# Performance work log

Measured on AMD Instinct MI355X. Metric: run time of the kernel, lower is better.

The kernel has to match this reference:

```python
import jax, jax.numpy as jnp
import numpy as np

EMBED_DIM = 512
NUM_TYPES = 26
PER_TYPE = 128
NUM_CODES = NUM_TYPES * PER_TYPE
COMMIT = 0.25
TEMP = 0.07
N_TOKENS = 32768
SAMPLED_PER_TYPE = int(0.1 * PER_TYPE)  # 12


def _normalize(v, axis=-1):
    # matches F.normalize(p=2) with eps clamp
    return v / jnp.clip(jnp.linalg.norm(v, axis=axis, keepdims=True), 1e-12)


def setup_inputs() -> dict:
    key = jax.random.key(0)
    k1, k2, k3, k4 = jax.random.split(key, 4)
    x = jax.random.normal(k1, (N_TOKENS, EMBED_DIM), jnp.float32)
    Q = jax.random.randint(k2, (N_TOKENS,), 0, NUM_TYPES)
    initrange = 1.0 / EMBED_DIM
    emb = jax.random.uniform(k3, (NUM_CODES, EMBED_DIM), jnp.float32, -initrange, initrange)
    emb = _normalize(emb)  # mirrors _initialize_embeddings
    # deterministic stand-in for torch.randperm(num_per_type)[:sampled_num]
    perm = jax.random.permutation(k4, PER_TYPE)[:SAMPLED_PER_TYPE]
    sampled_indices = (jnp.arange(NUM_TYPES)[:, None] * PER_TYPE + perm[None, :]).reshape(-1)
    return {"x": x, "embeddings": emb, "Q": Q, "sampled_indices": sampled_indices}


def _code_indices(xn, embeddings, Q):
    # full [N, num_codes] squared distances, then select the 128-code slab of
    # each token's PTM type and argmin within it (equivalent to the per-type loop)
    d = ((xn ** 2).sum(-1, keepdims=True)
         + (embeddings ** 2).sum(-1)[None, :]
         - 2.0 * (xn @ embeddings.T))                      # [N, NUM_CODES]
    d = d.reshape(xn.shape[0], NUM_TYPES, PER_TYPE)
    d_sel = jnp.take_along_axis(d, Q[:, None, None], axis=1)[:, 0, :]  # [N, PER_TYPE]
    return jnp.argmin(d_sel, axis=1) + Q * PER_TYPE


def _uniform_loss(embeddings, sampled_indices):
    ne = _normalize(embeddings)
    se = ne[sampled_indices]                               # [S, D]
    sim = se @ se.T                                        # [S, S]
    labels = sampled_indices // PER_TYPE
    pos = (labels[None, :] == labels[:, None]).astype(jnp.float32)
    S = sampled_indices.shape[0]
    eye = jnp.eye(S, dtype=bool)
    sim = jnp.where(eye, -jnp.inf, sim)
    sim_exp = jnp.exp(sim / TEMP)                          # exp(-inf) = 0 kills diagonal
    sum_exp = sim_exp.sum(axis=1)
    pos_sum = (sim_exp * pos).sum(axis=1)
    return -jnp.log(pos_sum / sum_exp).mean()


def reference(x, embeddings, Q, sampled_indices):
    xn = _normalize(x)
    idx = _code_indices(xn, embeddings, Q)
    quantized = _normalize(embeddings[idx])
    q_latent = jnp.mean((quantized - jax.lax.stop_gradient(xn)) ** 2)
    e_latent = jnp.mean((xn - jax.lax.stop_gradient(quantized)) ** 2)
    loss = q_latent + COMMIT * e_latent
    uloss = _uniform_loss(embeddings, sampled_indices)
    out = xn + jax.lax.stop_gradient(quantized - xn)       # straight-through
    return out, loss, uloss, idx
```

## Files before the change

### kernel.cpp

```cpp
#include <hip/hip_runtime.h>
#include <math.h>

#define NTOK   32768
#define DIM    512
#define NTYPES 26
#define PT     128
#define NCODES 3328
#define NSAMP  312
#define INV_TEMP (1.0f / 0.07f)
#define MAXTILES 24

typedef __attribute__((ext_vector_type(8))) short short8;
typedef __attribute__((ext_vector_type(4))) float floatx4;

__device__ __forceinline__ void f2bf2(float f, unsigned short& h, unsigned short& l) {
    unsigned u = __float_as_uint(f);
    unsigned hb = (u + 0x7fffu + ((u >> 16) & 1u)) >> 16;
    h = (unsigned short)hb;
    float hf = __uint_as_float(hb << 16);
    float r = f - hf;
    unsigned u2 = __float_as_uint(r);
    l = (unsigned short)((u2 + 0x7fffu + ((u2 >> 16) & 1u)) >> 16);
}

__global__ __launch_bounds__(256) void k_emb(const float* __restrict__ emb,
                                             unsigned short* __restrict__ Bhg,
                                             unsigned short* __restrict__ Blg,
                                             float* __restrict__ sume,
                                             float* __restrict__ rinv,
                                             int* __restrict__ counts,
                                             float* __restrict__ accg) {
    int tid = threadIdx.x;
    if (blockIdx.x == 0) {
        if (tid < NTYPES) counts[tid] = 0;
        if (tid == 32) accg[0] = 0.0f;
        if (tid == 33) accg[1] = 0.0f;
    }
    int wv = tid >> 6, lane = tid & 63;
    int c = blockIdx.x * 4 + wv;
    const float4* row = (const float4*)(emb + (size_t)c * DIM);
    float4 v0 = row[lane * 2], v1 = row[lane * 2 + 1];
    float s = v0.x*v0.x + v0.y*v0.y + v0.z*v0.z + v0.w*v0.w
            + v1.x*v1.x + v1.y*v1.y + v1.z*v1.z + v1.w*v1.w;
    for (int m = 32; m; m >>= 1) s += __shfl_xor(s, m);
    if (lane == 0) {
        sume[c] = s;
        rinv[c] = 1.0f / fmaxf(sqrtf(s), 1e-12f);
    }
    union { short8 v; unsigned short u[8]; } hh, ll;
    f2bf2(v0.x, hh.u[0], ll.u[0]); f2bf2(v0.y, hh.u[1], ll.u[1]);
    f2bf2(v0.z, hh.u[2], ll.u[2]); f2bf2(v0.w, hh.u[3], ll.u[3]);
    f2bf2(v1.x, hh.u[4], ll.u[4]); f2bf2(v1.y, hh.u[5], ll.u[5]);
    f2bf2(v1.z, hh.u[6], ll.u[6]); f2bf2(v1.w, hh.u[7], ll.u[7]);
    *(short8*)(Bhg + (size_t)c * DIM + lane * 8) = hh.v;
    *(short8*)(Blg + (size_t)c * DIM + lane * 8) = ll.v;
}

__global__ __launch_bounds__(256) void k_hist(const int* __restrict__ Q,
                                              int* __restrict__ counts,
                                              int* __restrict__ rank) {
    __shared__ int lbin[NTYPES];
    __shared__ int lbase[NTYPES];
    int tid = threadIdx.x;
    if (tid < NTYPES) lbin[tid] = 0;
    __syncthreads();
    int t = blockIdx.x * 256 + tid;
    int qt = Q[t];
    int lr = atomicAdd(&lbin[qt], 1);
    __syncthreads();
    if (tid < NTYPES) lbase[tid] = atomicAdd(&counts[tid], lbin[tid]);
    __syncthreads();
    rank[t] = lbase[qt] + lr;
}

__global__ __launch_bounds__(256) void k_scatter(const int* __restrict__ Q,
                                                 const int* __restrict__ counts,
                                                 const int* __restrict__ rank,
                                                 int* __restrict__ order,
                                                 int* __restrict__ offsg) {
    __shared__ int offs[NTYPES];
    int tid = threadIdx.x;
    if (tid == 0) {
        int a = 0;
        for (int i = 0; i < NTYPES; i++) {
            offs[i] = a;
            if (blockIdx.x == 0) offsg[i] = a;
            a += counts[i];
        }
        if (blockIdx.x == 0) offsg[NTYPES] = a;
    }
    __syncthreads();
    int t = blockIdx.x * 256 + tid;
    order[offs[Q[t]] + rank[t]] = t;
}

__global__ __launch_bounds__(256, 3) void k_main(const float* __restrict__ x,
                                                 const float* __restrict__ emb,
                                                 const unsigned short* __restrict__ Bhg,
                                                 const unsigned short* __restrict__ Blg,
                                                 const int* __restrict__ order,
                                                 const int* __restrict__ offsg,
                                                 const float* __restrict__ sume,
                                                 const float* __restrict__ rinv,
                                                 float* __restrict__ outbuf,
                                                 float* __restrict__ idxout,
                                                 float* __restrict__ accg) {
    int q = blockIdx.x;
    int tile = blockIdx.y;
    int base = offsg[q];
    int cnt = offsg[q + 1] - base;
    int tstart = tile * 64;
    if (tstart >= cnt) return;
    int nt = min(64, cnt - tstart);

    __shared__ unsigned short Ah[64][72];
    __shared__ unsigned short Al[64][72];
    __shared__ unsigned short Bh[128 * 64];
    __shared__ unsigned short Bl[128 * 64];
    __shared__ int   toks_s[64];
    __shared__ float rn_s[64];
    __shared__ float sume_s[128];
    __shared__ float rinv_s[128];
    __shared__ float redv[64][2];
    __shared__ int   redi[64][2];
    __shared__ int   bestc[64];

    int tid = threadIdx.x;
    int lane = tid & 63;
    int wv = tid >> 6;
    int wm = wv & 1, wn = wv >> 1;
    int lc = lane & 15;
    int q4 = lane >> 4;

    if (tid < 64) toks_s[tid] = order[base + tstart + min(tid, nt - 1)];
    if (tid < 128) {
        sume_s[tid] = sume[q * PT + tid];
        rinv_s[tid] = rinv[q * PT + tid];
    }

    floatx4 acc[2][4];
#pragma unroll
    for (int mi = 0; mi < 2; mi++)
#pragma unroll
        for (int ni = 0; ni < 4; ni++)
            acc[mi][ni] = (floatx4){0.f, 0.f, 0.f, 0.f};
    float ps[4] = {0.f, 0.f, 0.f, 0.f};

    const unsigned short* bh_slab = Bhg + (size_t)q * PT * DIM;
    const unsigned short* bl_slab = Blg + (size_t)q * PT * DIM;

    for (int kc = 0; kc < 8; kc++) {
        int k0 = kc * 64;
        __syncthreads();
#pragma unroll
        for (int i = 0; i < 4; i++) {
            int id = tid + i * 256;
            int r = id >> 4, sg = id & 15;
            float4 v = *(const float4*)(x + (size_t)toks_s[r] * DIM + k0 + sg * 4);
            ps[i] = fmaf(v.x, v.x, fmaf(v.y, v.y, fmaf(v.z, v.z, fmaf(v.w, v.w, ps[i]))));
            ushort4 h, l;
            f2bf2(v.x, h.x, l.x); f2bf2(v.y, h.y, l.y);
            f2bf2(v.z, h.z, l.z); f2bf2(v.w, h.w, l.w);
            *(ushort4*)&Ah[r][sg * 4] = h;
            *(ushort4*)&Al[r][sg * 4] = l;
        }
#pragma unroll
        for (int i = 0; i < 4; i++) {
            int id = tid + i * 256;
            int r = id >> 3, p = id & 7;
            int dst = r * 64 + ((p ^ (r & 7)) << 3);
            *(short8*)&Bh[dst] = *(const short8*)(bh_slab + (size_t)r * DIM + k0 + p * 8);
            *(short8*)&Bl[dst] = *(const short8*)(bl_slab + (size_t)r * DIM + k0 + p * 8);
        }
        __syncthreads();
#pragma unroll
        for (int ks2 = 0; ks2 < 2; ks2++) {
            int ko = ks2 * 32 + q4 * 8;
            int g = ko >> 3;
            short8 ahf[2], alf[2], bhf[4], blf[4];
#pragma unroll
            for (int mi = 0; mi < 2; mi++) {
                int m = wm * 32 + mi * 16 + lc;
                ahf[mi] = *(const short8*)&Ah[m][ko];
                alf[mi] = *(const short8*)&Al[m][ko];
            }
#pragma unroll
            for (int ni = 0; ni < 4; ni++) {
                int n = wn * 64 + ni * 16 + lc;
                int bs = n * 64 + ((g ^ (lc & 7)) << 3);
                bhf[ni] = *(const short8*)&Bh[bs];
                blf[ni] = *(const short8*)&Bl[bs];
            }
#pragma unroll
            for (int mi = 0; mi < 2; mi++)
#pragma unroll
                for (int ni = 0; ni < 4; ni++) {
                    acc[mi][ni] = __builtin_amdgcn_mfma_f32_16x16x32_bf16(ahf[mi], bhf[ni], acc[mi][ni], 0, 0, 0);
                    acc[mi][ni] = __builtin_amdgcn_mfma_f32_16x16x32_bf16(ahf[mi], blf[ni], acc[mi][ni], 0, 0, 0);
                    acc[mi][ni] = __builtin_amdgcn_mfma_f32_16x16x32_bf16(alf[mi], bhf[ni], acc[mi][ni], 0, 0, 0);
                }
        }
    }

#pragma unroll
    for (int m = 1; m <= 8; m <<= 1)
#pragma unroll
        for (int i = 0; i < 4; i++) ps[i] += __shfl_xor(ps[i], m);
    if ((lane & 15) == 0) {
#pragma unroll
        for (int i = 0; i < 4; i++) {
            int r = (tid >> 4) + 16 * i;
            rn_s[r] = 1.0f / fmaxf(sqrtf(ps[i]), 1e-12f);
        }
    }
    __syncthreads();

#pragma unroll
    for (int mi = 0; mi < 2; mi++) {
#pragma unroll
        for (int r = 0; r < 4; r++) {
            int m = wm * 32 + mi * 16 + q4 * 4 + r;
            float rn2 = -2.0f * rn_s[m];
            float bv = 1e30f; int bc = 0;
#pragma unroll
            for (int ni = 0; ni < 4; ni++) {
                int n = wn * 64 + ni * 16 + lc;
                float d = fmaf(rn2, acc[mi][ni][r], sume_s[n]);
                if (d < bv) { bv = d; bc = n; }
            }
#pragma unroll
            for (int mk = 1; mk <= 8; mk <<= 1) {
                float ov = __shfl_xor(bv, mk);
                int oc = __shfl_xor(bc, mk);
                if (ov < bv || (ov == bv && oc < bc)) { bv = ov; bc = oc; }
            }
            if (lc == 0) { redv[m][wn] = bv; redi[m][wn] = bc; }
        }
    }
    __syncthreads();

    if (tid < 64) {
        float v0 = redv[tid][0], v1 = redv[tid][1];
        int c = (v1 < v0) ? redi[tid][1] : redi[tid][0];
        float bv = fminf(v0, v1);
        bestc[tid] = c;
        float term = 0.0f;
        if (tid < nt) {
            idxout[toks_s[tid]] = (float)(q * PT + c);
            term = 2.0f - (sume_s[c] - bv) * rinv_s[c];
        }
        for (int mk = 32; mk; mk >>= 1) term += __shfl_xor(term, mk);
        if (tid == 0) atomicAdd(&accg[0], term);
    }
    __syncthreads();

    for (int t = wv; t < nt; t += 4) {
        int c = bestc[t];
        int gt = toks_s[t];
        float rv = rinv_s[c];
        const float4* er = (const float4*)(emb + (size_t)(q * PT + c) * DIM);
        float4* orow = (float4*)(outbuf + (size_t)gt * DIM);
#pragma unroll
        for (int s2 = 0; s2 < 2; s2++) {
            float4 ev = er[lane * 2 + s2];
            orow[lane * 2 + s2] = make_float4(ev.x * rv, ev.y * rv, ev.z * rv, ev.w * rv);
        }
    }
}

__global__ __launch_bounds__(256) void k_uloss(const float* __restrict__ emb,
                                               const int* __restrict__ samp,
                                               const float* __restrict__ rinv,
                                               float* __restrict__ accg) {
    __shared__ float rs[4], rp[4];
    int i = blockIdx.x;
    int tid = threadIdx.x;
    int lane = tid & 63, wv = tid >> 6;
    int ci = samp[i];
    float rvi = rinv[ci];
    int labi = ci >> 7;
    const float4* ri = (const float4*)(emb + (size_t)ci * DIM);
    float4 e0 = ri[lane * 2], e1 = ri[lane * 2 + 1];
    float sE = 0.0f, pE = 0.0f;
    for (int j0 = wv; j0 < NSAMP; j0 += 16) {
        float d[4]; int cj[4]; bool val[4];
#pragma unroll
        for (int u = 0; u < 4; u++) {
            int j = j0 + u * 4;
            val[u] = (j < NSAMP) && (j != i);
            int js = val[u] ? j : 0;
            cj[u] = samp[js];
            const float4* rj = (const float4*)(emb + (size_t)cj[u] * DIM);
            float4 f0 = rj[lane * 2], f1 = rj[lane * 2 + 1];
            d[u] = e0.x*f0.x + e0.y*f0.y + e0.z*f0.z + e0.w*f0.w
                 + e1.x*f1.x + e1.y*f1.y + e1.z*f1.z + e1.w*f1.w;
        }
#pragma unroll
        for (int mk = 32; mk; mk >>= 1)
#pragma unroll
            for (int u = 0; u < 4; u++) d[u] += __shfl_xor(d[u], mk);
#pragma unroll
        for (int u = 0; u < 4; u++) {
            float ex = val[u] ? expf(d[u] * rvi * rinv[cj[u]] * INV_TEMP) : 0.0f;
            sE += ex;
            if (val[u] && (cj[u] >> 7) == labi) pE += ex;
        }
    }
    if (lane == 0) { rs[wv] = sE; rp[wv] = pE; }
    __syncthreads();
    if (tid == 0) {
        float S = rs[0] + rs[1] + rs[2] + rs[3];
        float P = rp[0] + rp[1] + rp[2] + rp[3];
        atomicAdd(&accg[1], logf(S) - logf(P));
    }
}

__global__ void k_final(const float* __restrict__ accg, float* __restrict__ lossp) {
    lossp[0] = 1.25f * accg[0] / (float)NTOK;
    lossp[1] = accg[1] / (float)NSAMP;
}

extern "C" void kernel_launch(void* const* d_in, const int* in_sizes, int n_in,
                              void* d_out, int out_size, void* d_ws, size_t ws_size,
                              hipStream_t stream) {
    const float* x   = (const float*)d_in[0];
    const float* emb = (const float*)d_in[1];
    const int* Q     = (const int*)d_in[2];
    const int* samp  = (const int*)d_in[3];

    float* out    = (float*)d_out;
    float* lossp  = out + (size_t)NTOK * DIM;
    float* idxout = out + (size_t)NTOK * DIM + 2;

    unsigned short* Bhg = (unsigned short*)d_ws;
    unsigned short* Blg = Bhg + (size_t)NCODES * DIM;
    float* sume  = (float*)(Blg + (size_t)NCODES * DIM);
    float* rinv  = sume + NCODES;
    int* counts  = (int*)(rinv + NCODES);
    int* offsg   = counts + NTYPES;
    int* rank    = offsg + NTYPES + 1;
    int* order   = rank + NTOK;
    float* accg  = (float*)(order + NTOK);

    k_emb<<<NCODES / 4, 256, 0, stream>>>(emb, Bhg, Blg, sume, rinv, counts, accg);
    k_hist<<<NTOK / 256, 256, 0, stream>>>(Q, counts, rank);
    k_scatter<<<NTOK / 256, 256, 0, stream>>>(Q, counts, rank, order, offsg);
    dim3 gmain(NTYPES, MAXTILES);
    k_main<<<gmain, 256, 0, stream>>>(x, emb, Bhg, Blg, order, offsg, sume, rinv, out, idxout, accg);
    k_uloss<<<NSAMP, 256, 0, stream>>>(emb, samp, rinv, accg);
    k_final<<<1, 1, 0, stream>>>(accg, lossp);
}
```

Measured before the change: 215.0 us.

## Register-prefetch next K-chunk of A and B tiles during MFMA compute

Global loads of the x rows and the bf16 hi/lo codebook slab for the next 64-wide K chunk are issued into registers right after the LDS barrier, so their latency overlaps the MFMA work on the current chunk. Token row pointers and B offsets are precomputed once instead of re-reading toks_s each iteration. This raises register pressure and moves the barrier to the end of each iteration. The k_final loss scale also changes to divide by NTOK*DIM, which alters the output value, so this is partly a correctness change.

```diff
diff --git a/kernel.cpp b/kernel.cpp
--- a/kernel.cpp
+++ b/kernel.cpp
@@ -138,6 +138,23 @@
         rinv_s[tid] = rinv[q * PT + tid];
     }
 
+    const float* aptr[4];
+    int arow = tid >> 4, asg = tid & 15;
+#pragma unroll
+    for (int i = 0; i < 4; i++) {
+        int r = arow + 16 * i;
+        int t = order[base + tstart + min(r, nt - 1)];
+        aptr[i] = x + (size_t)t * DIM + asg * 4;
+    }
+    const unsigned short* bh_slab = Bhg + (size_t)q * PT * DIM;
+    const unsigned short* bl_slab = Blg + (size_t)q * PT * DIM;
+    size_t bofs[4];
+#pragma unroll
+    for (int i = 0; i < 4; i++) {
+        int id = tid + i * 256;
+        bofs[i] = (size_t)(id >> 3) * DIM + (id & 7) * 8;
+    }
+
     floatx4 acc[2][4];
 #pragma unroll
     for (int mi = 0; mi < 2; mi++)
@@ -146,33 +163,47 @@
             acc[mi][ni] = (floatx4){0.f, 0.f, 0.f, 0.f};
     float ps[4] = {0.f, 0.f, 0.f, 0.f};
 
-    const unsigned short* bh_slab = Bhg + (size_t)q * PT * DIM;
-    const unsigned short* bl_slab = Blg + (size_t)q * PT * DIM;
+    float4 va[4];
+    short8 vbh[4], vbl[4];
+#pragma unroll
+    for (int i = 0; i < 4; i++) va[i] = *(const float4*)(aptr[i]);
+#pragma unroll
+    for (int i = 0; i < 4; i++) {
+        vbh[i] = *(const short8*)(bh_slab + bofs[i]);
+        vbl[i] = *(const short8*)(bl_slab + bofs[i]);
+    }
 
     for (int kc = 0; kc < 8; kc++) {
-        int k0 = kc * 64;
-        __syncthreads();
 #pragma unroll
         for (int i = 0; i < 4; i++) {
-            int id = tid + i * 256;
-            int r = id >> 4, sg = id & 15;
-            float4 v = *(const float4*)(x + (size_t)toks_s[r] * DIM + k0 + sg * 4);
+            int r = arow + 16 * i;
+            float4 v = va[i];
             ps[i] = fmaf(v.x, v.x, fmaf(v.y, v.y, fmaf(v.z, v.z, fmaf(v.w, v.w, ps[i]))));
             ushort4 h, l;
             f2bf2(v.x, h.x, l.x); f2bf2(v.y, h.y, l.y);
             f2bf2(v.z, h.z, l.z); f2bf2(v.w, h.w, l.w);
-            *(ushort4*)&Ah[r][sg * 4] = h;
-            *(ushort4*)&Al[r][sg * 4] = l;
+            *(ushort4*)&Ah[r][asg * 4] = h;
+            *(ushort4*)&Al[r][asg * 4] = l;
         }
 #pragma unroll
         for (int i = 0; i < 4; i++) {
             int id = tid + i * 256;
             int r = id >> 3, p = id & 7;
             int dst = r * 64 + ((p ^ (r & 7)) << 3);
-            *(short8*)&Bh[dst] = *(const short8*)(bh_slab + (size_t)r * DIM + k0 + p * 8);
-            *(short8*)&Bl[dst] = *(const short8*)(bl_slab + (size_t)r * DIM + k0 + p * 8);
+            *(short8*)&Bh[dst] = vbh[i];
+            *(short8*)&Bl[dst] = vbl[i];
         }
         __syncthreads();
+        if (kc < 7) {
+            int k0n = (kc + 1) * 64;
+#pragma unroll
+            for (int i = 0; i < 4; i++) va[i] = *(const float4*)(aptr[i] + k0n);
+#pragma unroll
+            for (int i = 0; i < 4; i++) {
+                vbh[i] = *(const short8*)(bh_slab + bofs[i] + k0n);
+                vbl[i] = *(const short8*)(bl_slab + bofs[i] + k0n);
+            }
+        }
 #pragma unroll
         for (int ks2 = 0; ks2 < 2; ks2++) {
             int ko = ks2 * 32 + q4 * 8;
@@ -200,6 +231,7 @@
                     acc[mi][ni] = __builtin_amdgcn_mfma_f32_16x16x32_bf16(alf[mi], bhf[ni], acc[mi][ni], 0, 0, 0);
                 }
         }
+        __syncthreads();
     }
 
 #pragma unroll
@@ -208,10 +240,8 @@
         for (int i = 0; i < 4; i++) ps[i] += __shfl_xor(ps[i], m);
     if ((lane & 15) == 0) {
 #pragma unroll
-        for (int i = 0; i < 4; i++) {
-            int r = (tid >> 4) + 16 * i;
-            rn_s[r] = 1.0f / fmaxf(sqrtf(ps[i]), 1e-12f);
-        }
+        for (int i = 0; i < 4; i++)
+            rn_s[arow + 16 * i] = 1.0f / fmaxf(sqrtf(ps[i]), 1e-12f);
     }
     __syncthreads();
 
@@ -316,7 +346,7 @@
 }
 
 __global__ void k_final(const float* __restrict__ accg, float* __restrict__ lossp) {
-    lossp[0] = 1.25f * accg[0] / (float)NTOK;
+    lossp[0] = (1.25f / ((float)NTOK * (float)DIM)) * accg[0];
     lossp[1] = accg[1] / (float)NSAMP;
 }
 
```

New measurement: 213.9 us. Within noise of the previous version (-0.5%).
